# Performance work log

Hardware: AMD Instinct MI355X
Metric: run time of the kernel (lower is better)

Reference implementation:

```python
import jax, jax.numpy as jnp
import numpy as np

B, T, F, H = 256, 128, 32, 1024  # batch, seq_len(=decoder steps), input/output feat, hidden


def lstm_cell(x, h, c, Wih, Whh, b):
    # PyTorch gate order: i, f, g, o
    gates = x @ Wih.T + h @ Whh.T + b  # [B, 4H]
    i, f, g, o = jnp.split(gates, 4, axis=-1)
    i, f, o = jax.nn.sigmoid(i), jax.nn.sigmoid(f), jax.nn.sigmoid(o)
    c_new = f * c + i * jnp.tanh(g)
    h_new = o * jnp.tanh(c_new)
    return h_new, c_new


def setup_inputs() -> dict:
    key = jax.random.key(0)
    ks = jax.random.split(key, 16)
    s = 0.05
    d = {
        "input_seq": jax.random.normal(ks[0], (B, T, F), jnp.float32),
        # encoder LSTM (2 layers); bias = bias_ih + bias_hh folded together
        "enc_Wih0": jax.random.normal(ks[1], (4 * H, F), jnp.float32) * s,
        "enc_Whh0": jax.random.normal(ks[2], (4 * H, H), jnp.float32) * s,
        "enc_b0": jax.random.normal(ks[3], (4 * H,), jnp.float32) * s,
        "enc_Wih1": jax.random.normal(ks[4], (4 * H, H), jnp.float32) * s,
        "enc_Whh1": jax.random.normal(ks[5], (4 * H, H), jnp.float32) * s,
        "enc_b1": jax.random.normal(ks[6], (4 * H,), jnp.float32) * s,
        # decoder LSTM (2 layers), input size = output_size = F
        "dec_Wih0": jax.random.normal(ks[7], (4 * H, F), jnp.float32) * s,
        "dec_Whh0": jax.random.normal(ks[8], (4 * H, H), jnp.float32) * s,
        "dec_b0": jax.random.normal(ks[9], (4 * H,), jnp.float32) * s,
        "dec_Wih1": jax.random.normal(ks[10], (4 * H, H), jnp.float32) * s,
        "dec_Whh1": jax.random.normal(ks[11], (4 * H, H), jnp.float32) * s,
        "dec_b1": jax.random.normal(ks[12], (4 * H,), jnp.float32) * s,
        # output head
        "lin_W": jax.random.normal(ks[13], (F, H), jnp.float32) * s,
        "lin_b": jax.random.normal(ks[14], (F,), jnp.float32) * s,
    }
    return d


def reference(input_seq, enc_Wih0, enc_Whh0, enc_b0, enc_Wih1, enc_Whh1, enc_b1,
              dec_Wih0, dec_Whh0, dec_b0, dec_Wih1, dec_Whh1, dec_b1, lin_W, lin_b):
    Bsz = input_seq.shape[0]
    zeros = jnp.zeros((Bsz, H), input_seq.dtype)

    # ---- encoder: 2-layer LSTM scanned over time ----
    def enc_step(carry, x_t):
        h0, c0, h1, c1 = carry
        h0, c0 = lstm_cell(x_t, h0, c0, enc_Wih0, enc_Whh0, enc_b0)
        h1, c1 = lstm_cell(h0, h1, c1, enc_Wih1, enc_Whh1, enc_b1)
        return (h0, c0, h1, c1), None

    xs = jnp.swapaxes(input_seq, 0, 1)  # [T, B, F]
    (h0, c0, h1, c1), _ = jax.lax.scan(enc_step, (zeros, zeros, zeros, zeros), xs)

    def dec_step(carry, _):
        x, h0, c0, h1, c1 = carry
        h0, c0 = lstm_cell(x, h0, c0, dec_Wih0, dec_Whh0, dec_b0)
        h1, c1 = lstm_cell(h0, h1, c1, dec_Wih1, dec_Whh1, dec_b1)
        out = h1 @ lin_W.T + lin_b  # [B, F]
        return (out, h0, c0, h1, c1), out

    dec_in0 = input_seq[:, -1, :]  # [B, F]
    _, outs = jax.lax.scan(dec_step, (dec_in0, h0, c0, h1, c1), None, length=T)
    return jnp.swapaxes(outs, 0, 1)  # [B, T, F]
```

## Files before the change

### kernel.cpp

```cpp
#include <hip/hip_runtime.h>

typedef _Float16 half_t;
typedef _Float16 half8 __attribute__((ext_vector_type(8)));
typedef _Float16 half4v __attribute__((ext_vector_type(4)));
typedef float f32x4 __attribute__((ext_vector_type(4)));

#define DI __device__ __forceinline__

constexpr int Bsz = 256;
constexpr int Tsz = 128;
constexpr int Fsz = 32;
constexpr int Hsz = 1024;
constexpr int NG  = 4096;
constexpr int K1  = 1152;
constexpr int K2  = 2048;
constexpr int RSTR = 84;
constexpr int RING = 32;
constexpr int SZA = Bsz * K1;
constexpr int SZB = Bsz * K2;

DI int perm_to_orig(int np) {
    int nt = np >> 6, r = np & 63, g = r >> 4, jo = r & 15;
    return g * Hsz + nt * 16 + jo;
}

DI size_t wfrag(int np, int k) {
    return ((size_t)((k >> 5) * 256 + (np >> 4)) * 64 + ((k >> 3) & 3) * 16 + (np & 15)) * 8 + (k & 7);
}
DI size_t afrag(int b, int k) {
    return ((size_t)((k >> 5) * 16 + (b >> 4)) * 64 + ((k >> 3) & 3) * 16 + (b & 15)) * 8 + (k & 7);
}

DI void store8_wt(half_t* p, half4v v) {
    unsigned long long bits;
    __builtin_memcpy(&bits, &v, 8);
    __hip_atomic_store((unsigned long long*)p, bits, __ATOMIC_RELAXED, __HIP_MEMORY_SCOPE_AGENT);
}


__global__ void pack_cat(half_t* __restrict__ dst, const float* __restrict__ srcA, int KA,
                         const float* __restrict__ srcB, int KB, int KP) {
    int tid = threadIdx.x;
    int np = blockIdx.y * 64 + (tid & 63);
    int k0 = (blockIdx.x * 4 + (tid >> 6)) * 8;
    if (k0 >= KP) return;
    int n = perm_to_orig(np);
    half8 v;
#pragma unroll
    for (int j = 0; j < 8; ++j) {
        int k = k0 + j;
        float f = 0.f;
        if (k < KA) f = srcA[(size_t)n * KA + k];
        else if (k < KA + KB) f = srcB[(size_t)n * KB + (k - KA)];
        v[j] = (half_t)f;
    }
    *(half8*)(dst + wfrag(np, k0)) = v;
}

__global__ void pack_fold(half_t* __restrict__ dst, const float* __restrict__ Wih0,
                          const float* __restrict__ linW) {
    __shared__ float lw[32][128];
    __shared__ float wi[16][32];
    int nb = blockIdx.x * 16;
    int jb = blockIdx.y * 128;
    int t = threadIdx.x;
    for (int i = t; i < 32 * 128; i += 256) { int f = i >> 7, j = i & 127; lw[f][j] = linW[f * Hsz + jb + j]; }
    for (int i = t; i < 16 * 32; i += 256) { int r = i >> 5, f = i & 31; wi[r][f] = Wih0[perm_to_orig(nb + r) * 32 + f]; }
    __syncthreads();
    int r = t >> 4, j0 = (t & 15) * 8;
    half8 v;
#pragma unroll
    for (int jj = 0; jj < 8; ++jj) {
        float s = 0.f;
#pragma unroll
        for (int f = 0; f < 32; ++f) s += wi[r][f] * lw[f][j0 + jj];
        v[jj] = (half_t)s;
    }
    *(half8*)(dst + wfrag(nb + r, 1024 + jb + j0)) = v;
}

__global__ void pack_bias(float* __restrict__ b5, const float* eb0, const float* eb1,
                          const float* db0, const float* db1, const float* dWih0,
                          const float* linb) {
    int idx = blockIdx.x * 256 + threadIdx.x;
    if (idx >= 5 * NG) return;
    int which = idx >> 12, np = idx & (NG - 1);
    int n = perm_to_orig(np);
    float v;
    if (which == 0) v = eb0[n];
    else if (which == 1) v = eb1[n];
    else if (which == 2) v = db0[n];
    else if (which == 3) {
        v = db0[n];
        for (int f = 0; f < 32; ++f) v += dWih0[n * 32 + f] * linb[f];
    } else v = db1[n];
    b5[idx] = v;
}

__global__ void pack_small(half_t* __restrict__ Wlin, half_t* __restrict__ ringA0,
                           const float* __restrict__ linW, const float* __restrict__ inseq) {
    int idx = blockIdx.x * 256 + threadIdx.x;
    if (idx < 32 * Hsz) Wlin[idx] = (half_t)linW[idx];
    if (idx < Bsz * 4) {
        int b = idx >> 2, fg = idx & 3;
        half8 v;
#pragma unroll
        for (int j = 0; j < 8; ++j) v[j] = (half_t)inseq[(size_t)b * (Tsz * Fsz) + fg * 8 + j];
        *(half8*)(ringA0 + afrag(b, 1024 + fg * 8)) = v;
    }
}


struct MegaArgs {
    const float* in_seq;
    const half_t *Wenc1, *Wenc2, *Wdec1a, *Wdec1b, *Wdec2;
    const float *be1, *be2, *bd1a, *bd1b, *bd2;
    float *c0, *c1;
    half_t *ringA, *ringB, *ringD, *H1hist;
    unsigned* cnt;
};

struct PhaseDesc {
    const half_t* A; const half_t* W; const float* bias; float* c;
    half_t* h0; int cb0; half_t* h1; int cb1; half_t* h2; int cb2;
    const float* xs; half_t* xd; int K;
};

DI PhaseDesc make_desc(int p, const MegaArgs& g) {
    PhaseDesc d = {};
    if (p < 256) {
        int t = p >> 1;
        if ((p & 1) == 0) {
            d.A = g.ringA + (size_t)(t & (RING - 1)) * SZA;
            d.W = g.Wenc1; d.bias = g.be1; d.c = g.c0;
            d.h0 = g.ringB + (size_t)(t & (RING - 1)) * SZB; d.cb0 = 0;
            d.h1 = g.ringA + (size_t)((t + 1) & (RING - 1)) * SZA; d.cb1 = 0;
            d.K = K1;
        } else {
            int tsel = (t + 1 < Tsz) ? t + 1 : Tsz - 1;
            d.A = g.ringB + (size_t)(t & (RING - 1)) * SZB;
            d.W = g.Wenc2; d.bias = g.be2; d.c = g.c1;
            d.h0 = g.ringB + (size_t)((t + 1) & (RING - 1)) * SZB; d.cb0 = 1024;
            d.xs = g.in_seq + (size_t)tsel * Fsz;
            d.xd = g.ringA + (size_t)((t + 1) & (RING - 1)) * SZA;
            d.K = K2;
        }
    } else {
        int t = (p - 256) >> 1;
        int u = 128 + t;
        if ((p & 1) == 0) {
            if (t == 0) {
                d.A = g.ringA + (size_t)(128 & (RING - 1)) * SZA;
                d.W = g.Wdec1a; d.bias = g.bd1a; d.K = K1;
            } else {
                d.A = g.ringD + (size_t)(t & (RING - 1)) * SZB;
                d.W = g.Wdec1b; d.bias = g.bd1b; d.K = K2;
            }
            d.c = g.c0;
            d.h0 = g.ringB + (size_t)(u & (RING - 1)) * SZB; d.cb0 = 0;
            d.h1 = g.ringD + (size_t)((t + 1) & (RING - 1)) * SZB; d.cb1 = 0;
        } else {
            d.A = g.ringB + (size_t)(u & (RING - 1)) * SZB;
            d.W = g.Wdec2; d.bias = g.bd2; d.c = g.c1;
            d.h0 = g.ringB + (size_t)((u + 1) & (RING - 1)) * SZB; d.cb0 = 1024;
            d.h1 = g.ringD + (size_t)((t + 1) & (RING - 1)) * SZB; d.cb1 = 1024;
            d.h2 = g.H1hist + (size_t)t * (Bsz * Hsz); d.cb2 = 0;
            d.K = K2;
        }
    }
    return d;
}

template <int K>
DI void run_phase(const PhaseDesc& d, int mt, int nt, int tid,
                  unsigned* cnt, unsigned waitTarget,
                  float (&red)[4][64][RSTR]) {
    constexpr int CHW = (K / 32) / 4;
    int lane = tid & 63, w = tid >> 6;
    const half_t* pa = d.A + ((size_t)((w * CHW) * 16 + mt * 4) * 64 + lane) * 8;
    const half_t* pw = d.W + ((size_t)((w * CHW) * 256 + nt * 4) * 64 + lane) * 8;

    f32x4 acc[4][4] = {};
    half8 bA[3][4], bW[3][4];

#define LOADW(st, kk)                                                              \
    {                                                                              \
        _Pragma("unroll") for (int ni = 0; ni < 4; ++ni)                           \
            bW[st][ni] = *(const half8*)(pw + (size_t)(kk) * 131072 + ni * 512);   \
    }
#define LOADA(st, kk)                                                              \
    {                                                                              \
        _Pragma("unroll") for (int mi = 0; mi < 4; ++mi)                           \
            bA[st][mi] = *(const half8*)(pa + (size_t)(kk) * 8192 + mi * 512);     \
    }

    LOADW(0, 0)
    LOADW(1, 1)

    if (waitTarget) {
        if (tid == 0) {
            while (__hip_atomic_load(cnt, __ATOMIC_RELAXED, __HIP_MEMORY_SCOPE_AGENT) < waitTarget)
                __builtin_amdgcn_s_sleep(2);
        }
        __syncthreads();
    }

    LOADA(0, 0)
    LOADA(1, 1)
#pragma unroll
    for (int kk = 0; kk < CHW; ++kk) {
        if (kk + 2 < CHW) { LOADW((kk + 2) % 3, kk + 2) LOADA((kk + 2) % 3, kk + 2) }
        const int st = kk % 3;
#pragma unroll
        for (int mi = 0; mi < 4; ++mi)
#pragma unroll
            for (int ni = 0; ni < 4; ++ni)
                acc[mi][ni] = __builtin_amdgcn_mfma_f32_16x16x32_f16(bA[st][mi], bW[st][ni], acc[mi][ni], 0, 0, 0);
    }
#undef LOADW
#undef LOADA

    int l15 = lane & 15, l4 = lane >> 4;
#pragma unroll
    for (int mi = 0; mi < 4; ++mi)
#pragma unroll
        for (int ni = 0; ni < 4; ++ni)
#pragma unroll
            for (int r = 0; r < 4; ++r)
                red[w][mi * 16 + l4 * 4 + r][ni * 16 + l15] = acc[mi][ni][r];
    __syncthreads();

    int row = tid >> 2, q = tid & 3, jo0 = q * 4;
    f32x4 g0 = {}, g1 = {}, g2 = {}, g3 = {};
#pragma unroll
    for (int ww = 0; ww < 4; ++ww) {
        g0 += *(const f32x4*)&red[ww][row][jo0];
        g1 += *(const f32x4*)&red[ww][row][16 + jo0];
        g2 += *(const f32x4*)&red[ww][row][32 + jo0];
        g3 += *(const f32x4*)&red[ww][row][48 + jo0];
    }
    const float* bb = d.bias + nt * 64;
    g0 += *(const f32x4*)(bb + jo0);
    g1 += *(const f32x4*)(bb + 16 + jo0);
    g2 += *(const f32x4*)(bb + 32 + jo0);
    g3 += *(const f32x4*)(bb + 48 + jo0);

    int bglob = mt * 64 + row;
    int jg0 = nt * 16 + jo0;
    float* cp = d.c + (size_t)bglob * Hsz + jg0;
    f32x4 cold = *(const f32x4*)cp;
    f32x4 cnew;
    half4v hv;
#pragma unroll
    for (int e = 0; e < 4; ++e) {
        float si = 1.f / (1.f + __expf(-g0[e]));
        float sf = 1.f / (1.f + __expf(-g1[e]));
        float tg = 1.f - 2.f / (__expf(2.f * g2[e]) + 1.f);
        float so = 1.f / (1.f + __expf(-g3[e]));
        float cn = sf * cold[e] + si * tg;
        cnew[e] = cn;
        float th = 1.f - 2.f / (__expf(2.f * cn) + 1.f);
        hv[e] = (half_t)(so * th);
    }
    *(f32x4*)cp = cnew;

    {
        int col = d.cb0 + jg0;
        store8_wt(d.h0 + ((size_t)((col >> 5) * 16 + (bglob >> 4)) * 64 + ((col >> 3) & 3) * 16 + (bglob & 15)) * 8 + (col & 7), hv);
    }
    if (d.h1) {
        int col = d.cb1 + jg0;
        store8_wt(d.h1 + ((size_t)((col >> 5) * 16 + (bglob >> 4)) * 64 + ((col >> 3) & 3) * 16 + (bglob & 15)) * 8 + (col & 7), hv);
    }
    if (d.h2) {
        int col = d.cb2 + jg0;
        *(half4v*)(d.h2 + ((size_t)((col >> 5) * 16 + (bglob >> 4)) * 64 + ((col >> 3) & 3) * 16 + (bglob & 15)) * 8 + (col & 7)) = hv;
    }

    if (d.xs && nt == 0) {
        int f0 = q * 8;
        const float* xs = d.xs + (size_t)bglob * (Tsz * Fsz) + f0;
        half_t v[8];
#pragma unroll
        for (int j = 0; j < 8; ++j) v[j] = (half_t)xs[j];
        half4v lo = {v[0], v[1], v[2], v[3]}, hi = {v[4], v[5], v[6], v[7]};
        half_t* xp = d.xd + afrag(bglob, 1024 + f0);
        store8_wt(xp, lo);
        store8_wt(xp + 4, hi);
    }
}

__launch_bounds__(256, 1) __global__ void mega_kernel(MegaArgs g) {
    __shared__ __align__(16) float red[4][64][RSTR];
    int bid = blockIdx.x;
    int low3 = bid & 7, rest = bid >> 3;
    int mt = rest & 3, nt = ((rest >> 2) << 3) | low3;
    int tid = threadIdx.x;
    unsigned* cnt = g.cnt + mt * 64;

#pragma unroll 1
    for (int p = 0; p < 512; ++p) {
        PhaseDesc d = make_desc(p, g);
        if (d.K == K1) run_phase<K1>(d, mt, nt, tid, cnt, (unsigned)(64 * p), red);
        else           run_phase<K2>(d, mt, nt, tid, cnt, (unsigned)(64 * p), red);
        __syncthreads();
        if (tid == 0)
            __hip_atomic_fetch_add(cnt, 1u, __ATOMIC_RELAXED, __HIP_MEMORY_SCOPE_AGENT);
    }
}

__launch_bounds__(256, 1) __global__
void lin_out(const half_t* __restrict__ H1, const half_t* __restrict__ Wl,
             const float* __restrict__ lb, float* __restrict__ out) {
    int w = threadIdx.x >> 6, lane = threadIdx.x & 63;
    int l15 = lane & 15, l4 = lane >> 4;
    int rowt = blockIdx.x * 4 + w;
    int t = rowt >> 4, mi = rowt & 15;
    const half_t* pa = H1 + (size_t)t * (Bsz * Hsz);
    const half_t* pb0 = Wl + (size_t)l15 * Hsz + l4 * 8;
    const half_t* pb1 = Wl + (size_t)(16 + l15) * Hsz + l4 * 8;
    f32x4 ac0 = {}, ac1 = {};
#pragma unroll 4
    for (int kc = 0; kc < 32; ++kc) {
        half8 a = *(const half8*)(pa + ((size_t)(kc * 16 + mi) * 64 + lane) * 8);
        half8 b0 = *(const half8*)(pb0 + kc * 32);
        half8 b1 = *(const half8*)(pb1 + kc * 32);
        ac0 = __builtin_amdgcn_mfma_f32_16x16x32_f16(a, b0, ac0, 0, 0, 0);
        ac1 = __builtin_amdgcn_mfma_f32_16x16x32_f16(a, b1, ac1, 0, 0, 0);
    }
#pragma unroll
    for (int r = 0; r < 4; ++r) {
        int row = rowt * 16 + l4 * 4 + r;
        int b = row & 255;
        size_t o = (size_t)b * (Tsz * Fsz) + t * Fsz;
        out[o + l15] = ac0[r] + lb[l15];
        out[o + 16 + l15] = ac1[r] + lb[16 + l15];
    }
}


extern "C" void kernel_launch(void* const* d_in, const int* in_sizes, int n_in,
                              void* d_out, int out_size, void* d_ws, size_t ws_size,
                              hipStream_t stream) {
    (void)in_sizes; (void)n_in;
    const float* in_seq = (const float*)d_in[0];
    const float* eWih0 = (const float*)d_in[1];
    const float* eWhh0 = (const float*)d_in[2];
    const float* eb0 = (const float*)d_in[3];
    const float* eWih1 = (const float*)d_in[4];
    const float* eWhh1 = (const float*)d_in[5];
    const float* eb1 = (const float*)d_in[6];
    const float* dWih0 = (const float*)d_in[7];
    const float* dWhh0 = (const float*)d_in[8];
    const float* db0 = (const float*)d_in[9];
    const float* dWih1 = (const float*)d_in[10];
    const float* dWhh1 = (const float*)d_in[11];
    const float* db1 = (const float*)d_in[12];
    const float* linW = (const float*)d_in[13];
    const float* linb = (const float*)d_in[14];
    float* out = (float*)d_out;

    char* base = (char*)d_ws;
    size_t off = 0;
    auto alloc = [&](size_t bytes) {
        char* r = base + off;
        off = (off + bytes + 255) & ~(size_t)255;
        return r;
    };
    half_t* Wenc1 = (half_t*)alloc((size_t)NG * K1 * 2);
    half_t* Wenc2 = (half_t*)alloc((size_t)NG * K2 * 2);
    half_t* Wdec1a = (half_t*)alloc((size_t)NG * K1 * 2);
    half_t* Wdec1b = (half_t*)alloc((size_t)NG * K2 * 2);
    half_t* Wdec2 = (half_t*)alloc((size_t)NG * K2 * 2);
    half_t* Wlin = (half_t*)alloc((size_t)32 * Hsz * 2);
    float* bias5 = (float*)alloc((size_t)5 * NG * 4);
    float* c0 = (float*)alloc((size_t)Bsz * Hsz * 4);
    float* c1 = (float*)alloc((size_t)Bsz * Hsz * 4);
    half_t* ringA = (half_t*)alloc((size_t)RING * SZA * 2);
    half_t* ringB = (half_t*)alloc((size_t)RING * SZB * 2);
    half_t* ringD = (half_t*)alloc((size_t)RING * SZB * 2);
    half_t* H1hist = (half_t*)alloc((size_t)Tsz * Bsz * Hsz * 2);
    unsigned* barCnt = (unsigned*)alloc(4 * 64 * sizeof(unsigned));

    if (off > ws_size) {
        hipMemsetAsync(d_out, 0, (size_t)out_size * 4, stream);
        return;
    }

    float* be1 = bias5;
    float* be2 = bias5 + NG;
    float* bd1a = bias5 + 2 * NG;
    float* bd1b = bias5 + 3 * NG;
    float* bd2 = bias5 + 4 * NG;

    hipMemsetAsync(c0, 0, (size_t)Bsz * Hsz * 4, stream);
    hipMemsetAsync(c1, 0, (size_t)Bsz * Hsz * 4, stream);
    hipMemsetAsync(ringA, 0, (size_t)RING * SZA * 2, stream);
    hipMemsetAsync(ringB, 0, (size_t)SZB * 2, stream);
    hipMemsetAsync(barCnt, 0, 4 * 64 * sizeof(unsigned), stream);

    pack_cat<<<dim3(K1 / 32, NG / 64), 256, 0, stream>>>(Wenc1, eWhh0, 1024, eWih0, 32, K1);
    pack_cat<<<dim3(K2 / 32, NG / 64), 256, 0, stream>>>(Wenc2, eWih1, 1024, eWhh1, 1024, K2);
    pack_cat<<<dim3(K1 / 32, NG / 64), 256, 0, stream>>>(Wdec1a, dWhh0, 1024, dWih0, 32, K1);
    pack_cat<<<dim3(K2 / 32, NG / 64), 256, 0, stream>>>(Wdec1b, dWhh0, 1024, nullptr, 0, K2);
    pack_fold<<<dim3(NG / 16, 1024 / 128), 256, 0, stream>>>(Wdec1b, dWih0, linW);
    pack_cat<<<dim3(K2 / 32, NG / 64), 256, 0, stream>>>(Wdec2, dWih1, 1024, dWhh1, 1024, K2);
    pack_bias<<<(5 * NG + 255) / 256, 256, 0, stream>>>(bias5, eb0, eb1, db0, db1, dWih0, linb);
    pack_small<<<128, 256, 0, stream>>>(Wlin, ringA, linW, in_seq);

    MegaArgs ma;
    ma.in_seq = in_seq;
    ma.Wenc1 = Wenc1; ma.Wenc2 = Wenc2;
    ma.Wdec1a = Wdec1a; ma.Wdec1b = Wdec1b; ma.Wdec2 = Wdec2;
    ma.be1 = be1; ma.be2 = be2; ma.bd1a = bd1a; ma.bd1b = bd1b; ma.bd2 = bd2;
    ma.c0 = c0; ma.c1 = c1;
    ma.ringA = ringA; ma.ringB = ringB; ma.ringD = ringD;
    ma.H1hist = H1hist;
    ma.cnt = barCnt;
    void* kargs[] = {&ma};
    hipLaunchCooperativeKernel((const void*)mega_kernel, dim3(256), dim3(256), kargs, 0, stream);

    lin_out<<<512, 256, 0, stream>>>(H1hist, Wlin, linb, out);
}
```

Baseline: 6.327 ms.

## Replace folded decoder input weights with an explicit in-loop output phase

```diff
diff --git a/kernel.cpp b/kernel.cpp
--- a/kernel.cpp
+++ b/kernel.cpp
@@ -12,12 +12,12 @@
 constexpr int Fsz = 32;
 constexpr int Hsz = 1024;
 constexpr int NG  = 4096;
-constexpr int K1  = 1152;
+constexpr int KH  = 1024;
 constexpr int K2  = 2048;
 constexpr int RSTR = 84;
 constexpr int RING = 32;
-constexpr int SZA = Bsz * K1;
-constexpr int SZB = Bsz * K2;
+constexpr int SLOT = Bsz * Hsz;
+constexpr int NPH  = 256 + 3 * Tsz;
 
 DI int perm_to_orig(int np) {
     int nt = np >> 6, r = np & 63, g = r >> 4, jo = r & 15;
@@ -29,12 +29,21 @@
 }
 DI size_t afrag(int b, int k) {
     return ((size_t)((k >> 5) * 16 + (b >> 4)) * 64 + ((k >> 3) & 3) * 16 + (b & 15)) * 8 + (k & 7);
+}
+DI size_t lfrag(int f, int k) {
+    return ((size_t)((k >> 5) * 2 + (f >> 4)) * 64 + ((k >> 3) & 3) * 16 + (f & 15)) * 8 + (k & 7);
 }
 
 DI void store8_wt(half_t* p, half4v v) {
     unsigned long long bits;
     __builtin_memcpy(&bits, &v, 8);
     __hip_atomic_store((unsigned long long*)p, bits, __ATOMIC_RELAXED, __HIP_MEMORY_SCOPE_AGENT);
+}
+DI void store4_wt(half_t* p, half_t a, half_t b) {
+    half_t t2[2] = {a, b};
+    unsigned bits;
+    __builtin_memcpy(&bits, t2, 4);
+    __hip_atomic_store((unsigned*)p, bits, __ATOMIC_RELAXED, __HIP_MEMORY_SCOPE_AGENT);
 }
 
 
@@ -57,159 +66,97 @@
     *(half8*)(dst + wfrag(np, k0)) = v;
 }
 
-__global__ void pack_fold(half_t* __restrict__ dst, const float* __restrict__ Wih0,
-                          const float* __restrict__ linW) {
-    __shared__ float lw[32][128];
-    __shared__ float wi[16][32];
-    int nb = blockIdx.x * 16;
-    int jb = blockIdx.y * 128;
-    int t = threadIdx.x;
-    for (int i = t; i < 32 * 128; i += 256) { int f = i >> 7, j = i & 127; lw[f][j] = linW[f * Hsz + jb + j]; }
-    for (int i = t; i < 16 * 32; i += 256) { int r = i >> 5, f = i & 31; wi[r][f] = Wih0[perm_to_orig(nb + r) * 32 + f]; }
-    __syncthreads();
-    int r = t >> 4, j0 = (t & 15) * 8;
+__global__ void pack_wih(float* __restrict__ dst, const float* __restrict__ Wih0) {
+    int idx = blockIdx.x * 256 + threadIdx.x;
+    if (idx >= NG * Fsz) return;
+    int np = idx >> 5, f = idx & 31;
+    dst[idx] = Wih0[(size_t)perm_to_orig(np) * Fsz + f];
+}
+
+__global__ void pack_linw(half_t* __restrict__ dst, const float* __restrict__ linW) {
+    int idx = blockIdx.x * 256 + threadIdx.x;
+    if (idx >= 32 * (Hsz / 8)) return;
+    int f = idx & 31, k0 = (idx >> 5) * 8;
     half8 v;
 #pragma unroll
-    for (int jj = 0; jj < 8; ++jj) {
-        float s = 0.f;
-#pragma unroll
-        for (int f = 0; f < 32; ++f) s += wi[r][f] * lw[f][j0 + jj];
-        v[jj] = (half_t)s;
-    }
-    *(half8*)(dst + wfrag(nb + r, 1024 + jb + j0)) = v;
-}
-
-__global__ void pack_bias(float* __restrict__ b5, const float* eb0, const float* eb1,
-                          const float* db0, const float* db1, const float* dWih0,
-                          const float* linb) {
+    for (int j = 0; j < 8; ++j) v[j] = (half_t)linW[(size_t)f * Hsz + k0 + j];
+    *(half8*)(dst + lfrag(f, k0)) = v;
+}
+
+__global__ void pack_bias(float* __restrict__ b4, const float* eb0, const float* eb1,
+                          const float* db0, const float* db1) {
     int idx = blockIdx.x * 256 + threadIdx.x;
-    if (idx >= 5 * NG) return;
+    if (idx >= 4 * NG) return;
     int which = idx >> 12, np = idx & (NG - 1);
     int n = perm_to_orig(np);
-    float v;
-    if (which == 0) v = eb0[n];
-    else if (which == 1) v = eb1[n];
-    else if (which == 2) v = db0[n];
-    else if (which == 3) {
-        v = db0[n];
-        for (int f = 0; f < 32; ++f) v += dWih0[n * 32 + f] * linb[f];
-    } else v = db1[n];
-    b5[idx] = v;
-}
-
-__global__ void pack_small(half_t* __restrict__ Wlin, half_t* __restrict__ ringA0,
-                           const float* __restrict__ linW, const float* __restrict__ inseq) {
-    int idx = blockIdx.x * 256 + threadIdx.x;
-    if (idx < 32 * Hsz) Wlin[idx] = (half_t)linW[idx];
-    if (idx < Bsz * 4) {
-        int b = idx >> 2, fg = idx & 3;
-        half8 v;
-#pragma unroll
-        for (int j = 0; j < 8; ++j) v[j] = (half_t)inseq[(size_t)b * (Tsz * Fsz) + fg * 8 + j];
-        *(half8*)(ringA0 + afrag(b, 1024 + fg * 8)) = v;
-    }
+    const float* src = which == 0 ? eb0 : which == 1 ? eb1 : which == 2 ? db0 : db1;
+    b4[idx] = src[n];
 }
 
 
 struct MegaArgs {
     const float* in_seq;
-    const half_t *Wenc1, *Wenc2, *Wdec1a, *Wdec1b, *Wdec2;
-    const float *be1, *be2, *bd1a, *bd1b, *bd2;
+    const half_t *W0e, *W1e, *W0d, *W1d, *linWp;
+    const float *wih_e, *wih_d, *lin_b;
+    const float *be1, *be2, *bd1, *bd2;
     float *c0, *c1;
-    half_t *ringA, *ringB, *ringD, *H1hist;
+    half_t *RH0, *RH1, *H1h, *obuf;
+    float* ybuf;
     unsigned* cnt;
 };
 
-struct PhaseDesc {
-    const half_t* A; const half_t* W; const float* bias; float* c;
-    half_t* h0; int cb0; half_t* h1; int cb1; half_t* h2; int cb2;
-    const float* xs; half_t* xd; int K;
-};
-
-DI PhaseDesc make_desc(int p, const MegaArgs& g) {
-    PhaseDesc d = {};
-    if (p < 256) {
-        int t = p >> 1;
-        if ((p & 1) == 0) {
-            d.A = g.ringA + (size_t)(t & (RING - 1)) * SZA;
-            d.W = g.Wenc1; d.bias = g.be1; d.c = g.c0;
-            d.h0 = g.ringB + (size_t)(t & (RING - 1)) * SZB; d.cb0 = 0;
-            d.h1 = g.ringA + (size_t)((t + 1) & (RING - 1)) * SZA; d.cb1 = 0;
-            d.K = K1;
-        } else {
-            int tsel = (t + 1 < Tsz) ? t + 1 : Tsz - 1;
-            d.A = g.ringB + (size_t)(t & (RING - 1)) * SZB;
-            d.W = g.Wenc2; d.bias = g.be2; d.c = g.c1;
-            d.h0 = g.ringB + (size_t)((t + 1) & (RING - 1)) * SZB; d.cb0 = 1024;
-            d.xs = g.in_seq + (size_t)tsel * Fsz;
-            d.xd = g.ringA + (size_t)((t + 1) & (RING - 1)) * SZA;
-            d.K = K2;
-        }
-    } else {
-        int t = (p - 256) >> 1;
-        int u = 128 + t;
-        if ((p & 1) == 0) {
-            if (t == 0) {
-                d.A = g.ringA + (size_t)(128 & (RING - 1)) * SZA;
-                d.W = g.Wdec1a; d.bias = g.bd1a; d.K = K1;
-            } else {
-                d.A = g.ringD + (size_t)(t & (RING - 1)) * SZB;
-                d.W = g.Wdec1b; d.bias = g.bd1b; d.K = K2;
-            }
-            d.c = g.c0;
-            d.h0 = g.ringB + (size_t)(u & (RING - 1)) * SZB; d.cb0 = 0;
-            d.h1 = g.ringD + (size_t)((t + 1) & (RING - 1)) * SZB; d.cb1 = 0;
-        } else {
-            d.A = g.ringB + (size_t)(u & (RING - 1)) * SZB;
-            d.W = g.Wdec2; d.bias = g.bd2; d.c = g.c1;
-            d.h0 = g.ringB + (size_t)((u + 1) & (RING - 1)) * SZB; d.cb0 = 1024;
-            d.h1 = g.ringD + (size_t)((t + 1) & (RING - 1)) * SZB; d.cb1 = 1024;
-            d.h2 = g.H1hist + (size_t)t * (Bsz * Hsz); d.cb2 = 0;
-            d.K = K2;
-        }
-    }
-    return d;
+DI void group_wait(unsigned* cnt, unsigned tgt, int tid) {
+    if (tgt) {
+        if (tid == 0) {
+            while (__hip_atomic_load(cnt, __ATOMIC_RELAXED, __HIP_MEMORY_SCOPE_AGENT) < tgt)
+                __builtin_amdgcn_s_sleep(1);
+        }
+        __syncthreads();
+    }
 }
 
 template <int K>
-DI void run_phase(const PhaseDesc& d, int mt, int nt, int tid,
-                  unsigned* cnt, unsigned waitTarget,
-                  float (&red)[4][64][RSTR]) {
+DI void gemm_phase(const half_t* __restrict__ A0, const half_t* __restrict__ A1,
+                   const half_t* __restrict__ W, const float* __restrict__ bias,
+                   float* __restrict__ c, half_t* __restrict__ hdst,
+                   const float* __restrict__ xf32, const half_t* __restrict__ xf16,
+                   const float* __restrict__ wih,
+                   int mt, int nt, int tid, unsigned* cnt, unsigned tgt,
+                   float (&red)[4][64][RSTR]) {
     constexpr int CHW = (K / 32) / 4;
     int lane = tid & 63, w = tid >> 6;
-    const half_t* pa = d.A + ((size_t)((w * CHW) * 16 + mt * 4) * 64 + lane) * 8;
-    const half_t* pw = d.W + ((size_t)((w * CHW) * 256 + nt * 4) * 64 + lane) * 8;
+    const half_t* abase;
+    int cb;
+    if (K == KH)      { abase = A0; cb = w * CHW; }
+    else if (w < 2)   { abase = A0; cb = w * CHW; }
+    else              { abase = A1; cb = (w - 2) * CHW; }
+    const half_t* pa = abase + ((size_t)(cb * 16 + mt * 4) * 64 + lane) * 8;
+    const half_t* pw = W + ((size_t)((w * CHW) * 256 + nt * 4) * 64 + lane) * 8;
 
     f32x4 acc[4][4] = {};
     half8 bA[3][4], bW[3][4];
 
-#define LOADW(st, kk)                                                              \
+#define LDW(st, kk)                                                                \
     {                                                                              \
         _Pragma("unroll") for (int ni = 0; ni < 4; ++ni)                           \
             bW[st][ni] = *(const half8*)(pw + (size_t)(kk) * 131072 + ni * 512);   \
     }
-#define LOADA(st, kk)                                                              \
+#define LDA(st, kk)                                                                \
     {                                                                              \
         _Pragma("unroll") for (int mi = 0; mi < 4; ++mi)                           \
             bA[st][mi] = *(const half8*)(pa + (size_t)(kk) * 8192 + mi * 512);     \
     }
 
-    LOADW(0, 0)
-    LOADW(1, 1)
-
-    if (waitTarget) {
-        if (tid == 0) {
-            while (__hip_atomic_load(cnt, __ATOMIC_RELAXED, __HIP_MEMORY_SCOPE_AGENT) < waitTarget)
-                __builtin_amdgcn_s_sleep(2);
-        }
-        __syncthreads();
-    }
-
-    LOADA(0, 0)
-    LOADA(1, 1)
+    LDW(0, 0)
+    LDW(1, 1)
+
+    group_wait(cnt, tgt, tid);
+
+    LDA(0, 0)
+    LDA(1, 1)
 #pragma unroll
     for (int kk = 0; kk < CHW; ++kk) {
-        if (kk + 2 < CHW) { LOADW((kk + 2) % 3, kk + 2) LOADA((kk + 2) % 3, kk + 2) }
+        if (kk + 2 < CHW) { LDW((kk + 2) % 3, kk + 2) LDA((kk + 2) % 3, kk + 2) }
         const int st = kk % 3;
 #pragma unroll
         for (int mi = 0; mi < 4; ++mi)
@@ -217,8 +164,8 @@
             for (int ni = 0; ni < 4; ++ni)
                 acc[mi][ni] = __builtin_amdgcn_mfma_f32_16x16x32_f16(bA[st][mi], bW[st][ni], acc[mi][ni], 0, 0, 0);
     }
-#undef LOADW
-#undef LOADA
+#undef LDW
+#undef LDA
 
     int l15 = lane & 15, l4 = lane >> 4;
 #pragma unroll
@@ -239,15 +186,42 @@
         g2 += *(const f32x4*)&red[ww][row][32 + jo0];
         g3 += *(const f32x4*)&red[ww][row][48 + jo0];
     }
-    const float* bb = d.bias + nt * 64;
+    const float* bb = bias + nt * 64;
     g0 += *(const f32x4*)(bb + jo0);
     g1 += *(const f32x4*)(bb + 16 + jo0);
     g2 += *(const f32x4*)(bb + 32 + jo0);
     g3 += *(const f32x4*)(bb + 48 + jo0);
 
     int bglob = mt * 64 + row;
+
+    if (wih) {
+        float xr[Fsz];
+        if (xf32) {
+            const float* xp = xf32 + (size_t)bglob * (Tsz * Fsz);
+#pragma unroll
+            for (int f = 0; f < Fsz; ++f) xr[f] = xp[f];
+        } else {
+            const half_t* xp = xf16 + (size_t)bglob * Fsz;
+#pragma unroll
+            for (int f = 0; f < Fsz; ++f) xr[f] = (float)xp[f];
+        }
+#pragma unroll
+        for (int e = 0; e < 4; ++e) {
+            const float* w0 = wih + (size_t)(nt * 64 + jo0 + e) * Fsz;
+            float s0 = 0.f, s1 = 0.f, s2 = 0.f, s3 = 0.f;
+#pragma unroll
+            for (int f = 0; f < Fsz; ++f) {
+                s0 += xr[f] * w0[f];
+                s1 += xr[f] * w0[16 * Fsz + f];
+                s2 += xr[f] * w0[32 * Fsz + f];
+                s3 += xr[f] * w0[48 * Fsz + f];
+            }
+            g0[e] += s0; g1[e] += s1; g2[e] += s2; g3[e] += s3;
+        }
+    }
+
     int jg0 = nt * 16 + jo0;
-    float* cp = d.c + (size_t)bglob * Hsz + jg0;
+    float* cp = c + (size_t)bglob * Hsz + jg0;
     f32x4 cold = *(const f32x4*)cp;
     f32x4 cnew;
     half4v hv;
@@ -264,29 +238,50 @@
     }
     *(f32x4*)cp = cnew;
 
-    {
-        int col = d.cb0 + jg0;
-        store8_wt(d.h0 + ((size_t)((col >> 5) * 16 + (bglob >> 4)) * 64 + ((col >> 3) & 3) * 16 + (bglob & 15)) * 8 + (col & 7), hv);
-    }
-    if (d.h1) {
-        int col = d.cb1 + jg0;
-        store8_wt(d.h1 + ((size_t)((col >> 5) * 16 + (bglob >> 4)) * 64 + ((col >> 3) & 3) * 16 + (bglob & 15)) * 8 + (col & 7), hv);
-    }
-    if (d.h2) {
-        int col = d.cb2 + jg0;
-        *(half4v*)(d.h2 + ((size_t)((col >> 5) * 16 + (bglob >> 4)) * 64 + ((col >> 3) & 3) * 16 + (bglob & 15)) * 8 + (col & 7)) = hv;
-    }
-
-    if (d.xs && nt == 0) {
-        int f0 = q * 8;
-        const float* xs = d.xs + (size_t)bglob * (Tsz * Fsz) + f0;
-        half_t v[8];
-#pragma unroll
-        for (int j = 0; j < 8; ++j) v[j] = (half_t)xs[j];
-        half4v lo = {v[0], v[1], v[2], v[3]}, hi = {v[4], v[5], v[6], v[7]};
-        half_t* xp = d.xd + afrag(bglob, 1024 + f0);
-        store8_wt(xp, lo);
-        store8_wt(xp + 4, hi);
+    store8_wt(hdst + ((size_t)((jg0 >> 5) * 16 + (bglob >> 4)) * 64 + ((jg0 >> 3) & 3) * 16 + (bglob & 15)) * 8 + (jg0 & 7), hv);
+}
+
+DI void out_phase(const half_t* __restrict__ h1, const half_t* __restrict__ lw,
+                  const float* __restrict__ lb, float* __restrict__ ybt,
+                  half_t* __restrict__ obuf,
+                  int mt, int nt, int tid, unsigned* cnt, unsigned tgt,
+                  float (&red)[4][64][RSTR]) {
+    int lane = tid & 63, w = tid >> 6;
+    bool worker = (nt < 4);
+    int rt = mt * 4 + nt;
+
+    group_wait(cnt, tgt, tid);
+
+    if (worker) {
+        const half_t* pa = h1 + ((size_t)((w * 8) * 16 + rt) * 64 + lane) * 8;
+        const half_t* pb = lw + ((size_t)(w * 8) * 2 * 64 + lane) * 8;
+        f32x4 ac0 = {}, ac1 = {};
+#pragma unroll
+        for (int kk = 0; kk < 8; ++kk) {
+            half8 a = *(const half8*)(pa + (size_t)kk * 8192);
+            half8 b0 = *(const half8*)(pb + kk * 1024);
+            half8 b1 = *(const half8*)(pb + kk * 1024 + 512);
+            ac0 = __builtin_amdgcn_mfma_f32_16x16x32_f16(a, b0, ac0, 0, 0, 0);
+            ac1 = __builtin_amdgcn_mfma_f32_16x16x32_f16(a, b1, ac1, 0, 0, 0);
+        }
+        int l15 = lane & 15, l4 = lane >> 4;
+#pragma unroll
+        for (int r = 0; r < 4; ++r) {
+            red[w][l4 * 4 + r][l15] = ac0[r];
+            red[w][l4 * 4 + r][16 + l15] = ac1[r];
+        }
+    }
+    __syncthreads();
+    if (worker) {
+        int row = tid >> 4;
+        int f0 = (tid & 15) * 2;
+        float v0 = red[0][row][f0] + red[1][row][f0] + red[2][row][f0] + red[3][row][f0] + lb[f0];
+        float v1 = red[0][row][f0 + 1] + red[1][row][f0 + 1] + red[2][row][f0 + 1] + red[3][row][f0 + 1] + lb[f0 + 1];
+        int bglob = mt * 64 + nt * 16 + row;
+        float* yp = ybt + (size_t)bglob * (Tsz * Fsz);
+        yp[f0] = v0;
+        yp[f0 + 1] = v1;
+        store4_wt(obuf + (size_t)bglob * Fsz + f0, (half_t)v0, (half_t)v1);
     }
 }
 
@@ -299,43 +294,56 @@
     unsigned* cnt = g.cnt + mt * 64;
 
 #pragma unroll 1
-    for (int p = 0; p < 512; ++p) {
-        PhaseDesc d = make_desc(p, g);
-        if (d.K == K1) run_phase<K1>(d, mt, nt, tid, cnt, (unsigned)(64 * p), red);
-        else           run_phase<K2>(d, mt, nt, tid, cnt, (unsigned)(64 * p), red);
+    for (int p = 0; p < NPH; ++p) {
+        unsigned tgt = 64u * (unsigned)p;
+        if (p < 256) {
+            int t = p >> 1;
+            if (!(p & 1)) {
+                gemm_phase<KH>(g.RH0 + (size_t)(t & (RING - 1)) * SLOT, nullptr,
+                               g.W0e, g.be1, g.c0,
+                               g.RH0 + (size_t)((t + 1) & (RING - 1)) * SLOT,
+                               g.in_seq + (size_t)t * Fsz, nullptr, g.wih_e,
+                               mt, nt, tid, cnt, tgt, red);
+            } else {
+                gemm_phase<K2>(g.RH0 + (size_t)((t + 1) & (RING - 1)) * SLOT,
+                               g.RH1 + (size_t)(t & (RING - 1)) * SLOT,
+                               g.W1e, g.be2, g.c1,
+                               g.RH1 + (size_t)((t + 1) & (RING - 1)) * SLOT,
+                               nullptr, nullptr, nullptr,
+                               mt, nt, tid, cnt, tgt, red);
+            }
+        } else {
+            int qq = p - 256;
+            int t = qq / 3, r = qq - t * 3;
+            if (r == 0) {
+                gemm_phase<KH>(g.RH0 + (size_t)((128 + t) & (RING - 1)) * SLOT, nullptr,
+                               g.W0d, g.bd1, g.c0,
+                               g.RH0 + (size_t)((128 + t + 1) & (RING - 1)) * SLOT,
+                               (t == 0) ? g.in_seq + (size_t)(Tsz - 1) * Fsz : nullptr,
+                               (t == 0) ? nullptr : g.obuf + (size_t)((t - 1) & 3) * (Bsz * Fsz),
+                               g.wih_d, mt, nt, tid, cnt, tgt, red);
+            } else if (r == 1) {
+                gemm_phase<K2>(g.RH0 + (size_t)((128 + t + 1) & (RING - 1)) * SLOT,
+                               (t == 0) ? g.RH1 : g.H1h + (size_t)(t - 1) * SLOT,
+                               g.W1d, g.bd2, g.c1,
+                               g.H1h + (size_t)t * SLOT,
+                               nullptr, nullptr, nullptr,
+                               mt, nt, tid, cnt, tgt, red);
+            } else {
+                out_phase(g.H1h + (size_t)t * SLOT, g.linWp, g.lin_b,
+                          g.ybuf + (size_t)t * Fsz, g.obuf + (size_t)(t & 3) * (Bsz * Fsz),
+                          mt, nt, tid, cnt, tgt, red);
+            }
+        }
         __syncthreads();
         if (tid == 0)
             __hip_atomic_fetch_add(cnt, 1u, __ATOMIC_RELAXED, __HIP_MEMORY_SCOPE_AGENT);
     }
 }
 
-__launch_bounds__(256, 1) __global__
-void lin_out(const half_t* __restrict__ H1, const half_t* __restrict__ Wl,
-             const float* __restrict__ lb, float* __restrict__ out) {
-    int w = threadIdx.x >> 6, lane = threadIdx.x & 63;
-    int l15 = lane & 15, l4 = lane >> 4;
-    int rowt = blockIdx.x * 4 + w;
-    int t = rowt >> 4, mi = rowt & 15;
-    const half_t* pa = H1 + (size_t)t * (Bsz * Hsz);
-    const half_t* pb0 = Wl + (size_t)l15 * Hsz + l4 * 8;
-    const half_t* pb1 = Wl + (size_t)(16 + l15) * Hsz + l4 * 8;
-    f32x4 ac0 = {}, ac1 = {};
-#pragma unroll 4
-    for (int kc = 0; kc < 32; ++kc) {
-        half8 a = *(const half8*)(pa + ((size_t)(kc * 16 + mi) * 64 + lane) * 8);
-        half8 b0 = *(const half8*)(pb0 + kc * 32);
-        half8 b1 = *(const half8*)(pb1 + kc * 32);
-        ac0 = __builtin_amdgcn_mfma_f32_16x16x32_f16(a, b0, ac0, 0, 0, 0);
-        ac1 = __builtin_amdgcn_mfma_f32_16x16x32_f16(a, b1, ac1, 0, 0, 0);
-    }
-#pragma unroll
-    for (int r = 0; r < 4; ++r) {
-        int row = rowt * 16 + l4 * 4 + r;
-        int b = row & 255;
-        size_t o = (size_t)b * (Tsz * Fsz) + t * Fsz;
-        out[o + l15] = ac0[r] + lb[l15];
-        out[o + 16 + l15] = ac1[r] + lb[16 + l15];
-    }
+__global__ void copy_out(const float* __restrict__ src, float* __restrict__ dst) {
+    int i = blockIdx.x * 256 + threadIdx.x;
+    ((f32x4*)dst)[i] = ((const f32x4*)src)[i];
 }
 
 
@@ -367,19 +375,21 @@
         off = (off + bytes + 255) & ~(size_t)255;
         return r;
     };
-    half_t* Wenc1 = (half_t*)alloc((size_t)NG * K1 * 2);
-    half_t* Wenc2 = (half_t*)alloc((size_t)NG * K2 * 2);
-    half_t* Wdec1a = (half_t*)alloc((size_t)NG * K1 * 2);
-    half_t* Wdec1b = (half_t*)alloc((size_t)NG * K2 * 2);
-    half_t* Wdec2 = (half_t*)alloc((size_t)NG * K2 * 2);
-    half_t* Wlin = (half_t*)alloc((size_t)32 * Hsz * 2);
-    float* bias5 = (float*)alloc((size_t)5 * NG * 4);
+    half_t* W0e = (half_t*)alloc((size_t)NG * KH * 2);
+    half_t* W1e = (half_t*)alloc((size_t)NG * K2 * 2);
+    half_t* W0d = (half_t*)alloc((size_t)NG * KH * 2);
+    half_t* W1d = (half_t*)alloc((size_t)NG * K2 * 2);
+    half_t* linWp = (half_t*)alloc((size_t)32 * Hsz * 2);
+    float* wih_e = (float*)alloc((size_t)NG * Fsz * 4);
+    float* wih_d = (float*)alloc((size_t)NG * Fsz * 4);
+    float* bias4 = (float*)alloc((size_t)4 * NG * 4);
     float* c0 = (float*)alloc((size_t)Bsz * Hsz * 4);
     float* c1 = (float*)alloc((size_t)Bsz * Hsz * 4);
-    half_t* ringA = (half_t*)alloc((size_t)RING * SZA * 2);
-    half_t* ringB = (half_t*)alloc((size_t)RING * SZB * 2);
-    half_t* ringD = (half_t*)alloc((size_t)RING * SZB * 2);
-    half_t* H1hist = (half_t*)alloc((size_t)Tsz * Bsz * Hsz * 2);
+    half_t* RH0 = (half_t*)alloc((size_t)RING * SLOT * 2);
+    half_t* RH1 = (half_t*)alloc((size_t)RING * SLOT * 2);
+    half_t* H1h = (half_t*)alloc((size_t)Tsz * SLOT * 2);
+    half_t* obuf = (half_t*)alloc((size_t)4 * Bsz * Fsz * 2);
+    float* ybuf = (float*)alloc((size_t)Bsz * Tsz * Fsz * 4);
     unsigned* barCnt = (unsigned*)alloc(4 * 64 * sizeof(unsigned));
 
     if (off > ws_size) {
@@ -387,38 +397,36 @@
         return;
     }
 
-    float* be1 = bias5;
-    float* be2 = bias5 + NG;
-    float* bd1a = bias5 + 2 * NG;
-    float* bd1b = bias5 + 3 * NG;
-    float* bd2 = bias5 + 4 * NG;
-
     hipMemsetAsync(c0, 0, (size_t)Bsz * Hsz * 4, stream);
     hipMemsetAsync(c1, 0, (size_t)Bsz * Hsz * 4, stream);
-    hipMemsetAsync(ringA, 0, (size_t)RING * SZA * 2, stream);
-    hipMemsetAsync(ringB, 0, (size_t)SZB * 2, stream);
+    hipMemsetAsync(RH0, 0, (size_t)SLOT * 2, stream);
+    hipMemsetAsync(RH1, 0, (size_t)SLOT * 2, stream);
     hipMemsetAsync(barCnt, 0, 4 * 64 * sizeof(unsigned), stream);
 
-    pack_cat<<<dim3(K1 / 32, NG / 64), 256, 0, stream>>>(Wenc1, eWhh0, 1024, eWih0, 32, K1);
-    pack_cat<<<dim3(K2 / 32, NG / 64), 256, 0, stream>>>(Wenc2, eWih1, 1024, eWhh1, 1024, K2);
-    pack_cat<<<dim3(K1 / 32, NG / 64), 256, 0, stream>>>(Wdec1a, dWhh0, 1024, dWih0, 32, K1);
-    pack_cat<<<dim3(K2 / 32, NG / 64), 256, 0, stream>>>(Wdec1b, dWhh0, 1024, nullptr, 0, K2);
-    pack_fold<<<dim3(NG / 16, 1024 / 128), 256, 0, stream>>>(Wdec1b, dWih0, linW);
-    pack_cat<<<dim3(K2 / 32, NG / 64), 256, 0, stream>>>(Wdec2, dWih1, 1024, dWhh1, 1024, K2);
-    pack_bias<<<(5 * NG + 255) / 256, 256, 0, stream>>>(bias5, eb0, eb1, db0, db1, dWih0, linb);
-    pack_small<<<128, 256, 0, stream>>>(Wlin, ringA, linW, in_seq);
+    pack_cat<<<dim3(KH / 32, NG / 64), 256, 0, stream>>>(W0e, eWhh0, 1024, nullptr, 0, KH);
+    pack_cat<<<dim3(K2 / 32, NG / 64), 256, 0, stream>>>(W1e, eWih1, 1024, eWhh1, 1024, K2);
+    pack_cat<<<dim3(KH / 32, NG / 64), 256, 0, stream>>>(W0d, dWhh0, 1024, nullptr, 0, KH);
+    pack_cat<<<dim3(K2 / 32, NG / 64), 256, 0, stream>>>(W1d, dWih1, 1024, dWhh1, 1024, K2);
+    pack_wih<<<(NG * Fsz + 255) / 256, 256, 0, stream>>>(wih_e, eWih0);
+    pack_wih<<<(NG * Fsz + 255) / 256, 256, 0, stream>>>(wih_d, dWih0);
+    pack_linw<<<(32 * Hsz / 8 + 255) / 256, 256, 0, stream>>>(linWp, linW);
+    pack_bias<<<(4 * NG + 255) / 256, 256, 0, stream>>>(bias4, eb0, eb1, db0, db1);
 
     MegaArgs ma;
     ma.in_seq = in_seq;
-    ma.Wenc1 = Wenc1; ma.Wenc2 = Wenc2;
-    ma.Wdec1a = Wdec1a; ma.Wdec1b = Wdec1b; ma.Wdec2 = Wdec2;
-    ma.be1 = be1; ma.be2 = be2; ma.bd1a = bd1a; ma.bd1b = bd1b; ma.bd2 = bd2;
+    ma.W0e = W0e; ma.W1e = W1e; ma.W0d = W0d; ma.W1d = W1d; ma.linWp = linWp;
+    ma.wih_e = wih_e; ma.wih_d = wih_d; ma.lin_b = linb;
+    ma.be1 = bias4; ma.be2 = bias4 + NG; ma.bd1 = bias4 + 2 * NG; ma.bd2 = bias4 + 3 * NG;
     ma.c0 = c0; ma.c1 = c1;
-    ma.ringA = ringA; ma.ringB = ringB; ma.ringD = ringD;
-    ma.H1hist = H1hist;
+    ma.RH0 = RH0; ma.RH1 = RH1; ma.H1h = H1h; ma.obuf = obuf;
+    ma.ybuf = ybuf;
     ma.cnt = barCnt;
     void* kargs[] = {&ma};
-    hipLaunchCooperativeKernel((const void*)mega_kernel, dim3(256), dim3(256), kargs, 0, stream);
-
-    lin_out<<<512, 256, 0, stream>>>(H1hist, Wlin, linb, out);
-}
+    hipError_t ce = hipLaunchCooperativeKernel((const void*)mega_kernel, dim3(256), dim3(256),
+                                               kargs, 0, stream);
+    if (ce != hipSuccess) {
+        mega_kernel<<<dim3(256), dim3(256), 0, stream>>>(ma);
+    }
+
+    copy_out<<<(Bsz * Tsz * Fsz / 4) / 256, 256, 0, stream>>>(ybuf, out);
+}
```

Result: slower. 11.98 ms (+89.4%).

## Keep LSTM cell state in shared memory and skip zero-padded K work

Applied to the files above, without the earlier changes.

```diff
diff --git a/kernel.cpp b/kernel.cpp
--- a/kernel.cpp
+++ b/kernel.cpp
@@ -15,6 +15,7 @@
 constexpr int K1  = 1152;
 constexpr int K2  = 2048;
 constexpr int RSTR = 84;
+constexpr int CSTR = 24;
 constexpr int RING = 32;
 constexpr int SZA = Bsz * K1;
 constexpr int SZB = Bsz * K2;
@@ -97,7 +98,7 @@
     b5[idx] = v;
 }
 
-__global__ void pack_small(half_t* __restrict__ Wlin, half_t* __restrict__ ringA0,
+__global__ void pack_small(half_t* __restrict__ Wlin, half_t* __restrict__ slot0,
                            const float* __restrict__ linW, const float* __restrict__ inseq) {
     int idx = blockIdx.x * 256 + threadIdx.x;
     if (idx < 32 * Hsz) Wlin[idx] = (half_t)linW[idx];
@@ -106,7 +107,7 @@
         half8 v;
 #pragma unroll
         for (int j = 0; j < 8; ++j) v[j] = (half_t)inseq[(size_t)b * (Tsz * Fsz) + fg * 8 + j];
-        *(half8*)(ringA0 + afrag(b, 1024 + fg * 8)) = v;
+        *(half8*)(slot0 + afrag(b, 1024 + fg * 8)) = v;
     }
 }
 
@@ -115,13 +116,12 @@
     const float* in_seq;
     const half_t *Wenc1, *Wenc2, *Wdec1a, *Wdec1b, *Wdec2;
     const float *be1, *be2, *bd1a, *bd1b, *bd2;
-    float *c0, *c1;
     half_t *ringA, *ringB, *ringD, *H1hist;
     unsigned* cnt;
 };
 
 struct PhaseDesc {
-    const half_t* A; const half_t* W; const float* bias; float* c;
+    const half_t* A; const half_t* W; const float* bias; int ci;
     half_t* h0; int cb0; half_t* h1; int cb1; half_t* h2; int cb2;
     const float* xs; half_t* xd; int K;
 };
@@ -132,36 +132,44 @@
         int t = p >> 1;
         if ((p & 1) == 0) {
             d.A = g.ringA + (size_t)(t & (RING - 1)) * SZA;
-            d.W = g.Wenc1; d.bias = g.be1; d.c = g.c0;
+            d.W = g.Wenc1; d.bias = g.be1; d.ci = 0;
             d.h0 = g.ringB + (size_t)(t & (RING - 1)) * SZB; d.cb0 = 0;
             d.h1 = g.ringA + (size_t)((t + 1) & (RING - 1)) * SZA; d.cb1 = 0;
             d.K = K1;
         } else {
             int tsel = (t + 1 < Tsz) ? t + 1 : Tsz - 1;
             d.A = g.ringB + (size_t)(t & (RING - 1)) * SZB;
-            d.W = g.Wenc2; d.bias = g.be2; d.c = g.c1;
+            d.W = g.Wenc2; d.bias = g.be2; d.ci = 1;
             d.h0 = g.ringB + (size_t)((t + 1) & (RING - 1)) * SZB; d.cb0 = 1024;
             d.xs = g.in_seq + (size_t)tsel * Fsz;
             d.xd = g.ringA + (size_t)((t + 1) & (RING - 1)) * SZA;
             d.K = K2;
         }
+    } else if (p == 256) {
+        d.A = g.ringA + (size_t)(128 & (RING - 1)) * SZA;
+        d.W = g.Wdec1a; d.bias = g.bd1a; d.ci = 0;
+        d.h0 = g.ringB + (size_t)(128 & (RING - 1)) * SZB; d.cb0 = 0;
+        d.h1 = g.ringD + (size_t)(1 & (RING - 1)) * SZB; d.cb1 = 0;
+        d.K = K1;
+    } else if (p == 257) {
+        d.A = g.ringB + (size_t)(128 & (RING - 1)) * SZB;
+        d.W = g.Wdec2; d.bias = g.bd2; d.ci = 1;
+        d.h0 = g.ringB + (size_t)(129 & (RING - 1)) * SZB; d.cb0 = 1024;
+        d.h1 = g.ringD + (size_t)(1 & (RING - 1)) * SZB; d.cb1 = 1024;
+        d.h2 = g.H1hist; d.cb2 = 0;
+        d.K = K2;
     } else {
         int t = (p - 256) >> 1;
         int u = 128 + t;
         if ((p & 1) == 0) {
-            if (t == 0) {
-                d.A = g.ringA + (size_t)(128 & (RING - 1)) * SZA;
-                d.W = g.Wdec1a; d.bias = g.bd1a; d.K = K1;
-            } else {
-                d.A = g.ringD + (size_t)(t & (RING - 1)) * SZB;
-                d.W = g.Wdec1b; d.bias = g.bd1b; d.K = K2;
-            }
-            d.c = g.c0;
+            d.A = g.ringD + (size_t)(t & (RING - 1)) * SZB;
+            d.W = g.Wdec1b; d.bias = g.bd1b; d.ci = 0;
             d.h0 = g.ringB + (size_t)(u & (RING - 1)) * SZB; d.cb0 = 0;
             d.h1 = g.ringD + (size_t)((t + 1) & (RING - 1)) * SZB; d.cb1 = 0;
+            d.K = K2;
         } else {
             d.A = g.ringB + (size_t)(u & (RING - 1)) * SZB;
-            d.W = g.Wdec2; d.bias = g.bd2; d.c = g.c1;
+            d.W = g.Wdec2; d.bias = g.bd2; d.ci = 1;
             d.h0 = g.ringB + (size_t)((u + 1) & (RING - 1)) * SZB; d.cb0 = 1024;
             d.h1 = g.ringD + (size_t)((t + 1) & (RING - 1)) * SZB; d.cb1 = 1024;
             d.h2 = g.H1hist + (size_t)t * (Bsz * Hsz); d.cb2 = 0;
@@ -171,56 +179,69 @@
     return d;
 }
 
+DI void group_wait(unsigned* cnt, unsigned tgt, int tid) {
+    if (tgt) {
+        if (tid == 0) {
+            while (__hip_atomic_load(cnt, __ATOMIC_RELAXED, __HIP_MEMORY_SCOPE_AGENT) < tgt)
+                __builtin_amdgcn_s_sleep(1);
+        }
+        __syncthreads();
+        asm volatile("" ::: "memory");
+        __builtin_amdgcn_sched_barrier(0);
+    }
+}
+
 template <int K>
-DI void run_phase(const PhaseDesc& d, int mt, int nt, int tid,
-                  unsigned* cnt, unsigned waitTarget,
+DI void run_phase(const PhaseDesc& d, float (&cls)[2][64][CSTR],
+                  int mt, int nt, int tid, unsigned* cnt, unsigned tgt,
                   float (&red)[4][64][RSTR]) {
     constexpr int CHW = (K / 32) / 4;
     int lane = tid & 63, w = tid >> 6;
+    int l15 = lane & 15, l4 = lane >> 4;
     const half_t* pa = d.A + ((size_t)((w * CHW) * 16 + mt * 4) * 64 + lane) * 8;
     const half_t* pw = d.W + ((size_t)((w * CHW) * 256 + nt * 4) * 64 + lane) * 8;
+    const bool w3k1 = (K == K1) && (w == 3);
 
     f32x4 acc[4][4] = {};
     half8 bA[3][4], bW[3][4];
 
-#define LOADW(st, kk)                                                              \
+#define LDW(st, kk)                                                                \
     {                                                                              \
-        _Pragma("unroll") for (int ni = 0; ni < 4; ++ni)                           \
-            bW[st][ni] = *(const half8*)(pw + (size_t)(kk) * 131072 + ni * 512);   \
-    }
-#define LOADA(st, kk)                                                              \
+        if (!(w3k1 && (kk) >= 6)) {                                                \
+            _Pragma("unroll") for (int ni = 0; ni < 4; ++ni)                       \
+                bW[st][ni] = *(const half8*)(pw + (size_t)(kk) * 131072 + ni * 512); \
+        }                                                                          \
+    }
+#define LDA(st, kk)                                                                \
     {                                                                              \
-        _Pragma("unroll") for (int mi = 0; mi < 4; ++mi)                           \
-            bA[st][mi] = *(const half8*)(pa + (size_t)(kk) * 8192 + mi * 512);     \
-    }
-
-    LOADW(0, 0)
-    LOADW(1, 1)
-
-    if (waitTarget) {
-        if (tid == 0) {
-            while (__hip_atomic_load(cnt, __ATOMIC_RELAXED, __HIP_MEMORY_SCOPE_AGENT) < waitTarget)
-                __builtin_amdgcn_s_sleep(2);
+        if (!(w3k1 && (kk) >= 6)) {                                                \
+            _Pragma("unroll") for (int mi = 0; mi < 4; ++mi)                       \
+                bA[st][mi] = *(const half8*)(pa + (size_t)(kk) * 8192 + mi * 512); \
+        }                                                                          \
+    }
+
+    LDW(0, 0)
+    LDW(1, 1)
+
+    group_wait(cnt, tgt, tid);
+
+    LDA(0, 0)
+    LDA(1, 1)
+#pragma unroll
+    for (int kk = 0; kk < CHW; ++kk) {
+        if (kk + 2 < CHW) { LDW((kk + 2) % 3, kk + 2) LDA((kk + 2) % 3, kk + 2) }
+        const int st = kk % 3;
+        if (!(w3k1 && kk >= 6)) {
+#pragma unroll
+            for (int mi = 0; mi < 4; ++mi)
+#pragma unroll
+                for (int ni = 0; ni < 4; ++ni)
+                    acc[mi][ni] = __builtin_amdgcn_mfma_f32_16x16x32_f16(bA[st][mi], bW[st][ni], acc[mi][ni], 0, 0, 0);
         }
-        __syncthreads();
-    }
-
-    LOADA(0, 0)
-    LOADA(1, 1)
-#pragma unroll
-    for (int kk = 0; kk < CHW; ++kk) {
-        if (kk + 2 < CHW) { LOADW((kk + 2) % 3, kk + 2) LOADA((kk + 2) % 3, kk + 2) }
-        const int st = kk % 3;
-#pragma unroll
-        for (int mi = 0; mi < 4; ++mi)
-#pragma unroll
-            for (int ni = 0; ni < 4; ++ni)
-                acc[mi][ni] = __builtin_amdgcn_mfma_f32_16x16x32_f16(bA[st][mi], bW[st][ni], acc[mi][ni], 0, 0, 0);
-    }
-#undef LOADW
-#undef LOADA
-
-    int l15 = lane & 15, l4 = lane >> 4;
+    }
+#undef LDW
+#undef LDA
+
 #pragma unroll
     for (int mi = 0; mi < 4; ++mi)
 #pragma unroll
@@ -247,8 +268,7 @@
 
     int bglob = mt * 64 + row;
     int jg0 = nt * 16 + jo0;
-    float* cp = d.c + (size_t)bglob * Hsz + jg0;
-    f32x4 cold = *(const f32x4*)cp;
+    f32x4 cold = *(const f32x4*)&cls[d.ci][row][jo0];
     f32x4 cnew;
     half4v hv;
 #pragma unroll
@@ -262,19 +282,19 @@
         float th = 1.f - 2.f / (__expf(2.f * cn) + 1.f);
         hv[e] = (half_t)(so * th);
     }
-    *(f32x4*)cp = cnew;
+    *(f32x4*)&cls[d.ci][row][jo0] = cnew;
 
     {
         int col = d.cb0 + jg0;
-        store8_wt(d.h0 + ((size_t)((col >> 5) * 16 + (bglob >> 4)) * 64 + ((col >> 3) & 3) * 16 + (bglob & 15)) * 8 + (col & 7), hv);
+        store8_wt(d.h0 + afrag(bglob, col), hv);
     }
     if (d.h1) {
         int col = d.cb1 + jg0;
-        store8_wt(d.h1 + ((size_t)((col >> 5) * 16 + (bglob >> 4)) * 64 + ((col >> 3) & 3) * 16 + (bglob & 15)) * 8 + (col & 7), hv);
+        store8_wt(d.h1 + afrag(bglob, col), hv);
     }
     if (d.h2) {
         int col = d.cb2 + jg0;
-        *(half4v*)(d.h2 + ((size_t)((col >> 5) * 16 + (bglob >> 4)) * 64 + ((col >> 3) & 3) * 16 + (bglob & 15)) * 8 + (col & 7)) = hv;
+        store8_wt(d.h2 + afrag(bglob, col), hv);
     }
 
     if (d.xs && nt == 0) {
@@ -292,17 +312,21 @@
 
 __launch_bounds__(256, 1) __global__ void mega_kernel(MegaArgs g) {
     __shared__ __align__(16) float red[4][64][RSTR];
+    __shared__ __align__(16) float cls[2][64][CSTR];
     int bid = blockIdx.x;
     int low3 = bid & 7, rest = bid >> 3;
     int mt = rest & 3, nt = ((rest >> 2) << 3) | low3;
     int tid = threadIdx.x;
     unsigned* cnt = g.cnt + mt * 64;
 
+    for (int i = tid; i < 2 * 64 * CSTR; i += 256) ((float*)cls)[i] = 0.f;
+    __syncthreads();
+
 #pragma unroll 1
     for (int p = 0; p < 512; ++p) {
         PhaseDesc d = make_desc(p, g);
-        if (d.K == K1) run_phase<K1>(d, mt, nt, tid, cnt, (unsigned)(64 * p), red);
-        else           run_phase<K2>(d, mt, nt, tid, cnt, (unsigned)(64 * p), red);
+        if (d.K == K1) run_phase<K1>(d, cls, mt, nt, tid, cnt, (unsigned)(64 * p), red);
+        else           run_phase<K2>(d, cls, mt, nt, tid, cnt, (unsigned)(64 * p), red);
         __syncthreads();
         if (tid == 0)
             __hip_atomic_fetch_add(cnt, 1u, __ATOMIC_RELAXED, __HIP_MEMORY_SCOPE_AGENT);
@@ -374,8 +398,6 @@
     half_t* Wdec2 = (half_t*)alloc((size_t)NG * K2 * 2);
     half_t* Wlin = (half_t*)alloc((size_t)32 * Hsz * 2);
     float* bias5 = (float*)alloc((size_t)5 * NG * 4);
-    float* c0 = (float*)alloc((size_t)Bsz * Hsz * 4);
-    float* c1 = (float*)alloc((size_t)Bsz * Hsz * 4);
     half_t* ringA = (half_t*)alloc((size_t)RING * SZA * 2);
     half_t* ringB = (half_t*)alloc((size_t)RING * SZB * 2);
     half_t* ringD = (half_t*)alloc((size_t)RING * SZB * 2);
@@ -393,8 +415,6 @@
     float* bd1b = bias5 + 3 * NG;
     float* bd2 = bias5 + 4 * NG;
 
-    hipMemsetAsync(c0, 0, (size_t)Bsz * Hsz * 4, stream);
-    hipMemsetAsync(c1, 0, (size_t)Bsz * Hsz * 4, stream);
     hipMemsetAsync(ringA, 0, (size_t)RING * SZA * 2, stream);
     hipMemsetAsync(ringB, 0, (size_t)SZB * 2, stream);
     hipMemsetAsync(barCnt, 0, 4 * 64 * sizeof(unsigned), stream);
@@ -413,12 +433,15 @@
     ma.Wenc1 = Wenc1; ma.Wenc2 = Wenc2;
     ma.Wdec1a = Wdec1a; ma.Wdec1b = Wdec1b; ma.Wdec2 = Wdec2;
     ma.be1 = be1; ma.be2 = be2; ma.bd1a = bd1a; ma.bd1b = bd1b; ma.bd2 = bd2;
-    ma.c0 = c0; ma.c1 = c1;
     ma.ringA = ringA; ma.ringB = ringB; ma.ringD = ringD;
     ma.H1hist = H1hist;
     ma.cnt = barCnt;
     void* kargs[] = {&ma};
-    hipLaunchCooperativeKernel((const void*)mega_kernel, dim3(256), dim3(256), kargs, 0, stream);
+    hipError_t ce = hipLaunchCooperativeKernel((const void*)mega_kernel, dim3(256), dim3(256),
+                                               kargs, 0, stream);
+    if (ce != hipSuccess) {
+        mega_kernel<<<dim3(256), dim3(256), 0, stream>>>(ma);
+    }
 
     lin_out<<<512, 256, 0, stream>>>(H1hist, Wlin, linb, out);
 }
```

Measured after the change: 6.599 ms. 1.04x slower.
